# Performance work log

Hardware: AMD Instinct MI355X
Metric: run time of the kernel (lower is better)

## Reference

```python
import jax, jax.numpy as jnp
import numpy as np

EPS = 1e-5

def _layer_norm(x, gamma, beta):
    mu = jnp.mean(x, axis=-1, keepdims=True)
    var = jnp.var(x, axis=-1, keepdims=True)
    return (x - mu) * jax.lax.rsqrt(var + EPS) * gamma + beta

def setup_inputs() -> dict:
    key = jax.random.key(0)
    ks = jax.random.split(key, 4)
    B, T, D, H = 16, 2048, 1024, 1024
    s_in = 1.0 / np.sqrt(D)
    return {
        "x": jax.random.normal(ks[0], (B, T, D), dtype=jnp.float32),
        "c": jnp.zeros((B, H), dtype=jnp.float32),
        "W_lt": jax.random.uniform(ks[1], (H, D), jnp.float32, -s_in, s_in),
        "W_g": jax.random.uniform(ks[2], (2 * H, D), jnp.float32, -s_in, s_in),
        "b_g": jnp.zeros((2 * H,), dtype=jnp.float32),
        "gamma_g": jnp.ones((2 * H,), dtype=jnp.float32),
        "beta_g": jnp.zeros((2 * H,), dtype=jnp.float32),
        "gamma_a": jnp.ones((H,), dtype=jnp.float32),
        "beta_a": jnp.zeros((H,), dtype=jnp.float32),
    }

def reference(x, c, W_lt, W_g, b_g, gamma_g, beta_g, gamma_a, beta_a):
    H = W_lt.shape[0]
    # x: [B,T,D]
    x_tilde = jnp.einsum("btd,hd->bth", x, W_lt)            # [B,T,H]
    gate = jax.nn.sigmoid(_layer_norm(jnp.einsum("btd,gd->btg", x, W_g) + b_g, gamma_g, beta_g))
    f = gate[:, :, :H]                                        # forget gate [B,T,H]
    r = gate[:, :, H:]                                        # reset gate  [B,T,H]
    new_data = (1.0 - f) * x_tilde

    def step(c_prev, ft_nd):
        f_t, nd_t = ft_nd
        c_t = f_t * c_prev + nd_t
        return c_t, c_t

    # scan over time: move T to leading axis
    c_final, all_c = jax.lax.scan(step, c, (jnp.swapaxes(f, 0, 1), jnp.swapaxes(new_data, 0, 1)))
    all_c = jnp.swapaxes(all_c, 0, 1)                         # [B,T,H]
    h = r * jax.nn.sigmoid(_layer_norm(all_c, gamma_a, beta_a)) + (1.0 - r) * x
    return (h, c_final)
```

## Files before the change

kernel.cpp:

```cpp
#include <hip/hip_runtime.h>
#include <stdint.h>

typedef unsigned short u16;
typedef u16 us8 __attribute__((ext_vector_type(8)));
typedef uint32_t u32x8 __attribute__((ext_vector_type(8)));
typedef __bf16 bf16x8 __attribute__((ext_vector_type(8)));
typedef float f32x4 __attribute__((ext_vector_type(4)));

#define BB 16
#define TT 2048
#define HH 1024
#define MM 32768
#define NN 3072
#define KK 1024

__device__ __forceinline__ float b2f(u16 u) {
    union { uint32_t i; float f; } v; v.i = ((uint32_t)u) << 16; return v.f;
}
__device__ __forceinline__ u16 f2b(float f) {
    union { uint32_t i; float f; } v; v.f = f;
    uint32_t r = v.i + 0x7fffu + ((v.i >> 16) & 1u);
    return (u16)(r >> 16);
}
__device__ __forceinline__ float sigm(float z) {
    return 1.f / (1.f + __expf(-z));
}
__device__ __forceinline__ void load_lds16(const u16* g, u16* l) {
    __builtin_amdgcn_global_load_lds(
        (const __attribute__((address_space(1))) void*)g,
        (__attribute__((address_space(3))) void*)l, 16, 0, 0);
}

__global__ __launch_bounds__(256) void k_cvt(const float* __restrict__ x,
                                             const float* __restrict__ wlt,
                                             const float* __restrict__ wg,
                                             u16* __restrict__ xb,
                                             u16* __restrict__ wb) {
    long i = (long)(blockIdx.x * 256 + threadIdx.x) * 8;
    const float* s;
    u16* o;
    if (i < 33554432L) { s = x + i; o = xb + i; }
    else {
        long j = i - 33554432L;
        s = (j < 1048576L) ? (wlt + j) : (wg + (j - 1048576L));
        o = wb + j;
    }
    float4 a = *(const float4*)(s);
    float4 b = *(const float4*)(s + 4);
    us8 r;
    r[0] = f2b(a.x); r[1] = f2b(a.y); r[2] = f2b(a.z); r[3] = f2b(a.w);
    r[4] = f2b(b.x); r[5] = f2b(b.y); r[6] = f2b(b.z); r[7] = f2b(b.w);
    *(us8*)o = r;
}

__global__ __launch_bounds__(256) void k_gemm(const u16* __restrict__ A,
                                              const u16* __restrict__ W,
                                              u16* __restrict__ Y) {
    __shared__ u16 As[128 * 32];
    __shared__ u16 Bs[128 * 32];
    const int tid = threadIdx.x;
    const int lane = tid & 63;
    const int q = lane >> 4;
    const int l16 = lane & 15;
    const int w = tid >> 6;
    const int wm = (w >> 1) * 64, wn = (w & 1) * 64;
    const int bx = blockIdx.x, by = blockIdx.y;

    const int s0 = w * 128 + lane;
    const int s1 = w * 128 + 64 + lane;
    const u16* ag0 = A + (size_t)(by * 128 + (s0 >> 2)) * KK + (s0 & 3) * 8;
    const u16* ag1 = A + (size_t)(by * 128 + (s1 >> 2)) * KK + (s1 & 3) * 8;
    const u16* wg0 = W + (size_t)(bx * 128 + (s0 >> 2)) * KK + (s0 & 3) * 8;
    const u16* wg1 = W + (size_t)(bx * 128 + (s1 >> 2)) * KK + (s1 & 3) * 8;
    u16* al0 = As + w * 1024;
    u16* al1 = As + w * 1024 + 512;
    u16* bl0 = Bs + w * 1024;
    u16* bl1 = Bs + w * 1024 + 512;

    f32x4 zero = {0.f, 0.f, 0.f, 0.f};
    f32x4 acc[4][4];
#pragma unroll
    for (int i = 0; i < 4; i++)
#pragma unroll
        for (int j = 0; j < 4; j++) acc[i][j] = zero;

    for (int k0 = 0; k0 < KK; k0 += 32) {
        __syncthreads();
        load_lds16(ag0 + k0, al0);
        load_lds16(ag1 + k0, al1);
        load_lds16(wg0 + k0, bl0);
        load_lds16(wg1 + k0, bl1);
        __syncthreads();
        bf16x8 af[4], bv[4];
#pragma unroll
        for (int i = 0; i < 4; i++)
            af[i] = *(const bf16x8*)&As[(wm + i * 16 + l16) * 32 + q * 8];
#pragma unroll
        for (int j = 0; j < 4; j++)
            bv[j] = *(const bf16x8*)&Bs[(wn + j * 16 + l16) * 32 + q * 8];
#pragma unroll
        for (int i = 0; i < 4; i++)
#pragma unroll
            for (int j = 0; j < 4; j++)
                acc[i][j] = __builtin_amdgcn_mfma_f32_16x16x32_bf16(
                    af[i], bv[j], acc[i][j], 0, 0, 0);
    }

#pragma unroll
    for (int i = 0; i < 4; i++) {
#pragma unroll
        for (int rg = 0; rg < 4; rg++) {
            int row = by * 128 + wm + i * 16 + q * 4 + rg;
            u16* yp = Y + (size_t)row * NN + bx * 128 + wn + l16;
#pragma unroll
            for (int j = 0; j < 4; j++) yp[j * 16] = f2b(acc[i][j][rg]);
        }
    }
}

__global__ __launch_bounds__(256) void k_lnsig(const u16* __restrict__ Y,
                                               const float* __restrict__ bg,
                                               const float* __restrict__ gg,
                                               const float* __restrict__ bt,
                                               uint32_t* __restrict__ FN,
                                               u16* __restrict__ R) {
    const int row = blockIdx.x;
    const int t = threadIdx.x;
    const u16* yr = Y + (size_t)row * 3072;
    us8 gv = *(const us8*)(yr + 1024 + t * 8);
    float z[8];
    float s = 0.f, s2 = 0.f;
#pragma unroll
    for (int k = 0; k < 8; k++) {
        z[k] = b2f(gv[k]) + bg[t * 8 + k];
        s += z[k];
        s2 += z[k] * z[k];
    }
#pragma unroll
    for (int m = 1; m < 64; m <<= 1) {
        s += __shfl_xor(s, m);
        s2 += __shfl_xor(s2, m);
    }
    __shared__ float red[8];
    if ((t & 63) == 0) { red[t >> 6] = s; red[(t >> 6) + 4] = s2; }
    __syncthreads();
    s = red[0] + red[1] + red[2] + red[3];
    s2 = red[4] + red[5] + red[6] + red[7];
    const float mu = s * (1.f / 2048.f);
    const float inv = rsqrtf(s2 * (1.f / 2048.f) - mu * mu + 1e-5f);
    float gate[8];
#pragma unroll
    for (int k = 0; k < 8; k++)
        gate[k] = sigm((z[k] - mu) * inv * gg[t * 8 + k] + bt[t * 8 + k]);
    if (t < 128) {
        us8 xt = *(const us8*)(yr + t * 8);
        u32x8 fn;
#pragma unroll
        for (int k = 0; k < 8; k++) {
            u16 fb = f2b(gate[k]);
            u16 nb = f2b((1.f - gate[k]) * b2f(xt[k]));
            fn[k] = (uint32_t)fb | ((uint32_t)nb << 16);
        }
        *(u32x8*)(FN + (size_t)row * 1024 + t * 8) = fn;
    } else {
        us8 ro;
#pragma unroll
        for (int k = 0; k < 8; k++) ro[k] = f2b(gate[k]);
        *(us8*)(R + (size_t)row * 1024 + (t - 128) * 8) = ro;
    }
}

__global__ __launch_bounds__(256) void k_scan1(const uint32_t* __restrict__ FN,
                                               float2* __restrict__ agg) {
    int u = blockIdx.x * 256 + threadIdx.x;
    int h2 = u & 511;
    int chunk = (u >> 9) & 31;
    int b = u >> 14;
    size_t base = (size_t)(b * 2048 + chunk * 64) * 1024 + h2 * 2;
    float F0 = 1.f, N0 = 0.f, F1 = 1.f, N1 = 0.f;
#pragma unroll 4
    for (int i = 0; i < 64; i++) {
        uint2 v = *(const uint2*)(FN + base + (size_t)i * 1024);
        float f0 = b2f((u16)(v.x & 0xffffu)), n0 = b2f((u16)(v.x >> 16));
        float f1 = b2f((u16)(v.y & 0xffffu)), n1 = b2f((u16)(v.y >> 16));
        N0 = fmaf(f0, N0, n0); F0 *= f0;
        N1 = fmaf(f1, N1, n1); F1 *= f1;
    }
    float4 o = {F0, N0, F1, N1};
    *(float4*)&agg[(size_t)(b * 32 + chunk) * 1024 + h2 * 2] = o;
}

__global__ __launch_bounds__(256) void k_scan2(const float2* __restrict__ agg,
                                               const float* __restrict__ c0,
                                               float* __restrict__ P) {
    int u = blockIdx.x * 256 + threadIdx.x;
    int b = u >> 10, h = u & 1023;
    float c = c0[u];
#pragma unroll 4
    for (int k = 0; k < 32; k++) {
        size_t idx = (size_t)(b * 32 + k) * 1024 + h;
        P[idx] = c;
        float2 fn = agg[idx];
        c = fmaf(fn.x, c, fn.y);
    }
}

__global__ __launch_bounds__(512) void k_scanout(const uint32_t* __restrict__ FN,
                                                 const float* __restrict__ P,
                                                 const u16* __restrict__ R,
                                                 const u16* __restrict__ xb,
                                                 const float* __restrict__ ga,
                                                 const float* __restrict__ ba,
                                                 float* __restrict__ out,
                                                 float* __restrict__ cfin) {
    __shared__ float2 red[2][8];
    const int t = threadIdx.x;
    const int b = blockIdx.x >> 5, chunk = blockIdx.x & 31;
    const int h = t * 2;
    const int w = t >> 6, lane = t & 63;
    float2 cp = *(const float2*)&P[(size_t)(b * 32 + chunk) * 1024 + h];
    float c0 = cp.x, c1 = cp.y;
    const float g0 = ga[h], g1 = ga[h + 1];
    const float be0 = ba[h], be1 = ba[h + 1];
    const size_t base = (size_t)(b * 2048 + chunk * 64) * 1024 + h;
#pragma unroll 2
    for (int i = 0; i < 64; i++) {
        const size_t ro = base + (size_t)i * 1024;
        uint2 fn = *(const uint2*)(FN + ro);
        uint32_t rv = *(const uint32_t*)(R + ro);
        uint32_t xv = *(const uint32_t*)(xb + ro);
        c0 = fmaf(b2f((u16)(fn.x & 0xffffu)), c0, b2f((u16)(fn.x >> 16)));
        c1 = fmaf(b2f((u16)(fn.y & 0xffffu)), c1, b2f((u16)(fn.y >> 16)));
        float s = c0 + c1, s2 = c0 * c0 + c1 * c1;
#pragma unroll
        for (int m = 1; m < 64; m <<= 1) {
            s += __shfl_xor(s, m);
            s2 += __shfl_xor(s2, m);
        }
        const int p = i & 1;
        if (lane == 0) red[p][w] = make_float2(s, s2);
        __syncthreads();
        s = 0.f; s2 = 0.f;
#pragma unroll
        for (int k = 0; k < 8; k++) { float2 v = red[p][k]; s += v.x; s2 += v.y; }
        const float mu = s * (1.f / 1024.f);
        const float inv = rsqrtf(s2 * (1.f / 1024.f) - mu * mu + 1e-5f);
        const float sg0 = sigm((c0 - mu) * inv * g0 + be0);
        const float sg1 = sigm((c1 - mu) * inv * g1 + be1);
        const float r0 = b2f((u16)(rv & 0xffffu)), r1 = b2f((u16)(rv >> 16));
        const float x0 = b2f((u16)(xv & 0xffffu)), x1 = b2f((u16)(xv >> 16));
        float2 ho = {r0 * sg0 + (1.f - r0) * x0, r1 * sg1 + (1.f - r1) * x1};
        *(float2*)(out + ro) = ho;
    }
    if (chunk == 31) *(float2*)(cfin + b * 1024 + h) = make_float2(c0, c1);
}

extern "C" void kernel_launch(void* const* d_in, const int* in_sizes, int n_in,
                              void* d_out, int out_size, void* d_ws, size_t ws_size,
                              hipStream_t stream) {
    const float* x   = (const float*)d_in[0];
    const float* c0  = (const float*)d_in[1];
    const float* wlt = (const float*)d_in[2];
    const float* wg  = (const float*)d_in[3];
    const float* bg  = (const float*)d_in[4];
    const float* gg  = (const float*)d_in[5];
    const float* btg = (const float*)d_in[6];
    const float* ga  = (const float*)d_in[7];
    const float* ba  = (const float*)d_in[8];
    float* out = (float*)d_out;

    char* ws = (char*)d_ws;
    u16* xb      = (u16*)(ws);
    u16* wb      = (u16*)(ws + 67108864);
    u16* y       = (u16*)(ws + 73400320);
    uint32_t* FN = (uint32_t*)(ws + 274726912);
    u16* R       = (u16*)(ws + 408944640);
    float2* agg  = (float2*)(ws + 476053504);
    float* P     = (float*)(ws + 480247808);

    k_cvt<<<17920, 256, 0, stream>>>(x, wlt, wg, xb, wb);
    k_gemm<<<dim3(24, 256), 256, 0, stream>>>(xb, wb, y);
    k_lnsig<<<32768, 256, 0, stream>>>(y, bg, gg, btg, FN, R);
    k_scan1<<<1024, 256, 0, stream>>>(FN, agg);
    k_scan2<<<64, 256, 0, stream>>>(agg, c0, P);
    k_scanout<<<512, 512, 0, stream>>>(FN, P, R, xb, ga, ba, out,
                                       out + (size_t)33554432);
}
```

Before: 684.2 us.

## Rewrite GEMM with 256x256 tiles, double-buffered swizzled LDS and interleaved prefetch

Replaces the 128x128 single-stage GEMM with a 512-thread, 256x256x64 tile kernel. It double-buffers LDS with an XOR swizzle to avoid bank conflicts and issues global-to-LDS prefetches two k-steps ahead between MFMA phases. It also raises wave priority around MFMA bursts. The goal is to hide memory latency and raise MFMA utilisation in the dominant projection GEMM, at the cost of higher register and LDS use plus fragile hand-placed waitcnt and barrier logic.

```diff
diff --git a/kernel.cpp b/kernel.cpp
--- a/kernel.cpp
+++ b/kernel.cpp
@@ -13,6 +13,7 @@
 #define MM 32768
 #define NN 3072
 #define KK 1024
+#define NT 16
 
 __device__ __forceinline__ float b2f(u16 u) {
     union { uint32_t i; float f; } v; v.i = ((uint32_t)u) << 16; return v.f;
@@ -29,6 +30,9 @@
     __builtin_amdgcn_global_load_lds(
         (const __attribute__((address_space(1))) void*)g,
         (__attribute__((address_space(3))) void*)l, 16, 0, 0);
+}
+__device__ __forceinline__ f32x4 mf(bf16x8 a, bf16x8 b, f32x4 c) {
+    return __builtin_amdgcn_mfma_f32_16x16x32_bf16(a, b, c, 0, 0, 0);
 }
 
 __global__ __launch_bounds__(256) void k_cvt(const float* __restrict__ x,
@@ -53,67 +57,167 @@
     *(us8*)o = r;
 }
 
-__global__ __launch_bounds__(256) void k_gemm(const u16* __restrict__ A,
-                                              const u16* __restrict__ W,
-                                              u16* __restrict__ Y) {
-    __shared__ u16 As[128 * 32];
-    __shared__ u16 Bs[128 * 32];
+__global__ __launch_bounds__(512, 2) void k_gemm(const u16* __restrict__ A,
+                                                 const u16* __restrict__ W,
+                                                 u16* __restrict__ Y) {
+    __shared__ u16 As[2 * 16384];
+    __shared__ u16 Bs[2 * 16384];
     const int tid = threadIdx.x;
     const int lane = tid & 63;
+    const int w = tid >> 6;
+    const int wm = w >> 2;
+    const int wn = w & 3;
     const int q = lane >> 4;
     const int l16 = lane & 15;
-    const int w = tid >> 6;
-    const int wm = (w >> 1) * 64, wn = (w & 1) * 64;
-    const int bx = blockIdx.x, by = blockIdx.y;
-
-    const int s0 = w * 128 + lane;
-    const int s1 = w * 128 + 64 + lane;
-    const u16* ag0 = A + (size_t)(by * 128 + (s0 >> 2)) * KK + (s0 & 3) * 8;
-    const u16* ag1 = A + (size_t)(by * 128 + (s1 >> 2)) * KK + (s1 & 3) * 8;
-    const u16* wg0 = W + (size_t)(bx * 128 + (s0 >> 2)) * KK + (s0 & 3) * 8;
-    const u16* wg1 = W + (size_t)(bx * 128 + (s1 >> 2)) * KK + (s1 & 3) * 8;
-    u16* al0 = As + w * 1024;
-    u16* al1 = As + w * 1024 + 512;
-    u16* bl0 = Bs + w * 1024;
-    u16* bl1 = Bs + w * 1024 + 512;
+    const int bx = blockIdx.x;
+    const int by = blockIdx.y;
+
+    const int slog = ((tid & 7) ^ ((tid >> 3) & 7)) << 3;
+    const u16* aS = A + (size_t)(by * 256 + (tid >> 3)) * KK + slog;
+    const u16* bS = W + (size_t)(bx * 256 + ((tid >> 8) << 6) + ((tid >> 3) & 31)) * KK + slog;
+    u16* aD = As + w * 512;
+    u16* bD = Bs + w * 512;
+
+    load_lds16(aS,                aD);
+    load_lds16(aS + 128 * KK,     aD + 4096);
+    load_lds16(aS + 64 * KK,      aD + 8192);
+    load_lds16(aS + 192 * KK,     aD + 12288);
+    load_lds16(bS,                bD);
+    load_lds16(bS + 128 * KK,     bD + 4096);
+    load_lds16(bS + 32 * KK,      bD + 8192);
+    load_lds16(bS + 160 * KK,     bD + 12288);
+    load_lds16(aS + 64,           aD + 16384);
+    load_lds16(aS + 64 + 128*KK,  aD + 16384 + 4096);
+    load_lds16(aS + 64 + 64*KK,   aD + 16384 + 8192);
+    load_lds16(aS + 64 + 192*KK,  aD + 16384 + 12288);
+    load_lds16(bS + 64,           bD + 16384);
+    load_lds16(bS + 64 + 128*KK,  bD + 16384 + 4096);
+    load_lds16(bS + 64 + 32*KK,   bD + 16384 + 8192);
+    load_lds16(bS + 64 + 160*KK,  bD + 16384 + 12288);
+
+    const int key = l16 & 7;
+    const int sA0 = ((q ^ key) << 3);
+    const int sA1 = (((q ^ key) ^ 4) << 3);
+    const int aB0 = wm * 4096 + l16 * 64 + sA0;
+    const int aB1 = wm * 4096 + l16 * 64 + sA1;
+    const int bB0 = wn * 2048 + l16 * 64 + sA0;
+    const int bB1 = wn * 2048 + l16 * 64 + sA1;
 
     f32x4 zero = {0.f, 0.f, 0.f, 0.f};
-    f32x4 acc[4][4];
-#pragma unroll
-    for (int i = 0; i < 4; i++)
-#pragma unroll
-        for (int j = 0; j < 4; j++) acc[i][j] = zero;
-
-    for (int k0 = 0; k0 < KK; k0 += 32) {
-        __syncthreads();
-        load_lds16(ag0 + k0, al0);
-        load_lds16(ag1 + k0, al1);
-        load_lds16(wg0 + k0, bl0);
-        load_lds16(wg1 + k0, bl1);
-        __syncthreads();
-        bf16x8 af[4], bv[4];
-#pragma unroll
-        for (int i = 0; i < 4; i++)
-            af[i] = *(const bf16x8*)&As[(wm + i * 16 + l16) * 32 + q * 8];
-#pragma unroll
-        for (int j = 0; j < 4; j++)
-            bv[j] = *(const bf16x8*)&Bs[(wn + j * 16 + l16) * 32 + q * 8];
-#pragma unroll
-        for (int i = 0; i < 4; i++)
-#pragma unroll
-            for (int j = 0; j < 4; j++)
-                acc[i][j] = __builtin_amdgcn_mfma_f32_16x16x32_bf16(
-                    af[i], bv[j], acc[i][j], 0, 0, 0);
-    }
-
-#pragma unroll
-    for (int i = 0; i < 4; i++) {
-#pragma unroll
-        for (int rg = 0; rg < 4; rg++) {
-            int row = by * 128 + wm + i * 16 + q * 4 + rg;
-            u16* yp = Y + (size_t)row * NN + bx * 128 + wn + l16;
-#pragma unroll
-            for (int j = 0; j < 4; j++) yp[j * 16] = f2b(acc[i][j][rg]);
+    f32x4 acc[8][4];
+#pragma unroll
+    for (int i = 0; i < 8; ++i)
+#pragma unroll
+        for (int j = 0; j < 4; ++j) acc[i][j] = zero;
+    bf16x8 aR[4][2], bR[4][2];
+
+    asm volatile("s_waitcnt vmcnt(8)" ::: "memory");
+    __builtin_amdgcn_sched_barrier(0);
+    __builtin_amdgcn_s_barrier();
+    asm volatile("" ::: "memory");
+
+    for (int kt = 0; kt < NT; ++kt) {
+        const int cb = (kt & 1) << 14;
+        const int kc = (kt + 2) << 6;
+#pragma unroll
+        for (int i = 0; i < 4; ++i) {
+            aR[i][0] = *(const bf16x8*)&As[cb + i * 1024 + aB0];
+            aR[i][1] = *(const bf16x8*)&As[cb + i * 1024 + aB1];
+        }
+#pragma unroll
+        for (int f = 0; f < 4; ++f) {
+            bR[f][0] = *(const bf16x8*)&Bs[cb + (f >> 1) * 8192 + (f & 1) * 1024 + bB0];
+            bR[f][1] = *(const bf16x8*)&Bs[cb + (f >> 1) * 8192 + (f & 1) * 1024 + bB1];
+        }
+        asm volatile("" ::: "memory");
+        __builtin_amdgcn_s_barrier();
+        asm volatile("s_waitcnt lgkmcnt(0)" ::: "memory");
+        __builtin_amdgcn_sched_barrier(0);
+        __builtin_amdgcn_s_setprio(1);
+#pragma unroll
+        for (int i = 0; i < 4; ++i)
+#pragma unroll
+            for (int f = 0; f < 2; ++f) {
+                acc[i][f] = mf(aR[i][0], bR[f][0], acc[i][f]);
+                acc[i][f] = mf(aR[i][1], bR[f][1], acc[i][f]);
+            }
+        __builtin_amdgcn_s_setprio(0);
+        asm volatile("" ::: "memory");
+        __builtin_amdgcn_s_barrier();
+        asm volatile("" ::: "memory");
+        if (kt < NT - 2) {
+            load_lds16(aS + kc,            aD + cb);
+            load_lds16(aS + kc + 128*KK,   aD + cb + 4096);
+            load_lds16(bS + kc,            bD + cb);
+            load_lds16(bS + kc + 128*KK,   bD + cb + 4096);
+            load_lds16(bS + kc + 32*KK,    bD + cb + 8192);
+            load_lds16(bS + kc + 160*KK,   bD + cb + 12288);
+        }
+        asm volatile("" ::: "memory");
+        __builtin_amdgcn_s_barrier();
+        __builtin_amdgcn_s_setprio(1);
+#pragma unroll
+        for (int i = 0; i < 4; ++i)
+#pragma unroll
+            for (int f = 2; f < 4; ++f) {
+                acc[i][f] = mf(aR[i][0], bR[f][0], acc[i][f]);
+                acc[i][f] = mf(aR[i][1], bR[f][1], acc[i][f]);
+            }
+        __builtin_amdgcn_s_setprio(0);
+        asm volatile("" ::: "memory");
+        __builtin_amdgcn_s_barrier();
+        asm volatile("" ::: "memory");
+#pragma unroll
+        for (int i = 0; i < 4; ++i) {
+            aR[i][0] = *(const bf16x8*)&As[cb + 8192 + i * 1024 + aB0];
+            aR[i][1] = *(const bf16x8*)&As[cb + 8192 + i * 1024 + aB1];
+        }
+        asm volatile("" ::: "memory");
+        __builtin_amdgcn_s_barrier();
+        asm volatile("s_waitcnt lgkmcnt(0)" ::: "memory");
+        __builtin_amdgcn_sched_barrier(0);
+        __builtin_amdgcn_s_setprio(1);
+#pragma unroll
+        for (int i = 0; i < 4; ++i)
+#pragma unroll
+            for (int f = 0; f < 2; ++f) {
+                acc[4 + i][f] = mf(aR[i][0], bR[f][0], acc[4 + i][f]);
+                acc[4 + i][f] = mf(aR[i][1], bR[f][1], acc[4 + i][f]);
+            }
+        __builtin_amdgcn_s_setprio(0);
+        asm volatile("" ::: "memory");
+        __builtin_amdgcn_s_barrier();
+        asm volatile("" ::: "memory");
+        if (kt < NT - 2) {
+            load_lds16(aS + kc + 64*KK,    aD + cb + 8192);
+            load_lds16(aS + kc + 192*KK,   aD + cb + 12288);
+        }
+        asm volatile("" ::: "memory");
+        __builtin_amdgcn_s_barrier();
+        __builtin_amdgcn_s_setprio(1);
+#pragma unroll
+        for (int i = 0; i < 4; ++i)
+#pragma unroll
+            for (int f = 2; f < 4; ++f) {
+                acc[4 + i][f] = mf(aR[i][0], bR[f][0], acc[4 + i][f]);
+                acc[4 + i][f] = mf(aR[i][1], bR[f][1], acc[4 + i][f]);
+            }
+        __builtin_amdgcn_s_setprio(0);
+        if (kt < NT - 2) { asm volatile("s_waitcnt vmcnt(8)" ::: "memory"); }
+        else             { asm volatile("s_waitcnt vmcnt(0)" ::: "memory"); }
+        __builtin_amdgcn_sched_barrier(0);
+        __builtin_amdgcn_s_barrier();
+        asm volatile("" ::: "memory");
+    }
+
+#pragma unroll
+    for (int fm = 0; fm < 8; ++fm) {
+#pragma unroll
+        for (int rg = 0; rg < 4; ++rg) {
+            const int row = by * 256 + wm * 128 + fm * 16 + q * 4 + rg;
+            u16* yp = Y + (size_t)row * NN + bx * 256 + wn * 64 + l16;
+#pragma unroll
+            for (int fn = 0; fn < 4; ++fn) yp[fn * 16] = f2b(acc[fm][fn][rg]);
         }
     }
 }
@@ -279,7 +383,7 @@
     float* P     = (float*)(ws + 480247808);
 
     k_cvt<<<17920, 256, 0, stream>>>(x, wlt, wg, xb, wb);
-    k_gemm<<<dim3(24, 256), 256, 0, stream>>>(xb, wb, y);
+    k_gemm<<<dim3(NN / 256, MM / 256), 512, 0, stream>>>(xb, wb, y);
     k_lnsig<<<32768, 256, 0, stream>>>(y, bg, gg, btg, FN, R);
     k_scan1<<<1024, 256, 0, stream>>>(FN, agg);
     k_scan2<<<64, 256, 0, stream>>>(agg, c0, P);
```

Result: faster. 669.1 us (-2.2%).
